# Kernel optimization log

Measured on AMD Instinct MI355X. Metric: run time of the kernel, lower is better.

Reference implementation:

```python
import jax, jax.numpy as jnp
import numpy as np

IN_F = 512
OUT_F = 512
TREES = 50
DEPTH = 10  # levels above leaves; 2^DEPTH leaves per tree


def _build_forest(T, D):
    """Forest of T perfect binary trees. Nodes laid out level-by-level (leaves first).
    Returns node_order [N], adjacency [E,2] (parent, child; children consecutive,
    left then right, edges sorted by parent), edge_order [E]."""
    per = 2 ** (D + 1) - 1
    no = np.zeros(per, np.int64)
    adj_parts, eo_parts = [], []
    start, prev = 0, None
    for l in range(D + 1):
        n_l = 2 ** (D - l)
        idx = np.arange(start, start + n_l, dtype=np.int64)
        no[idx] = l
        if l > 0:
            parents = np.repeat(idx, 2)          # each parent twice
            adj_parts.append(np.stack([parents, prev], 1))  # prev = 2*n_l children, pairs consecutive
            eo_parts.append(np.full(2 * n_l, l, np.int64))
        prev, start = idx, start + n_l
    adj = np.concatenate(adj_parts, 0)
    eo = np.concatenate(eo_parts, 0)
    offs = np.arange(T, dtype=np.int64) * per
    node_order = np.tile(no, T)
    adjacency = (adj[None] + offs[:, None, None]).reshape(-1, 2)
    edge_order = np.tile(eo, T)
    return node_order, adjacency, edge_order


def setup_inputs() -> dict:
    key = jax.random.key(0)
    ks = jax.random.split(key, 8)
    no, adj, eo = _build_forest(TREES, DEPTH)
    N = no.shape[0]
    s_in = 1.0 / np.sqrt(IN_F).astype(np.float32)
    s_h = 1.0 / np.sqrt(OUT_F).astype(np.float32)
    return {
        "features": jax.random.normal(ks[0], (N, IN_F), jnp.float32),
        "node_order": jnp.asarray(no),
        "adjacency_list": jnp.asarray(adj),
        "edge_order": jnp.asarray(eo),
        "W_iou_w": jax.random.normal(ks[1], (3 * OUT_F, IN_F), jnp.float32) * s_in,
        "W_iou_b": jax.random.normal(ks[2], (3 * OUT_F,), jnp.float32) * s_in,
        "U_iou_l": jax.random.normal(ks[3], (3 * OUT_F, OUT_F), jnp.float32) * s_h,
        "U_iou_r": jax.random.normal(ks[4], (3 * OUT_F, OUT_F), jnp.float32) * s_h,
        "W_f_w": jax.random.normal(ks[5], (OUT_F, IN_F), jnp.float32) * s_in,
        "W_f_b": jax.random.normal(ks[6], (OUT_F,), jnp.float32) * s_in,
        "U_f_l": jax.random.normal(ks[7], (OUT_F, OUT_F), jnp.float32) * s_h,
        "U_f_r": jax.random.normal(jax.random.fold_in(key, 99), (OUT_F, OUT_F), jnp.float32) * s_h,
    }


def reference(features, node_order, adjacency_list, edge_order,
              W_iou_w, W_iou_b, U_iou_l, U_iou_r, W_f_w, W_f_b, U_f_l, U_f_r):
    # Tree topology is static integer data: hoist it to numpy so per-level index
    # sets are concrete (the original torch code host-syncs the same way).
    no = np.asarray(node_order)
    ao = np.asarray(adjacency_list)
    eo = np.asarray(edge_order)
    N, H = features.shape[0], W_f_w.shape[0]
    h = jnp.zeros((N, H), features.dtype)
    c = jnp.zeros((N, H), features.dtype)
    for l in range(int(no.max()) + 1):
        nodes = jnp.asarray(np.nonzero(no == l)[0])   # parents at this level, sorted
        x = features[nodes]                            # [P, F]
        if l == 0:
            iou = x @ W_iou_w.T + W_iou_b
            i, o, u = jnp.split(iou, 3, axis=1)
            c_new = jax.nn.sigmoid(i) * jnp.tanh(u)
        else:
            e = ao[eo == l]                            # [2P, 2]; children consecutive per parent
            p_rep = jnp.asarray(e[:, 0])               # parent repeated per child
            children = jnp.asarray(e[:, 1])
            ch = h[children]                           # [2P, H]
            cc = c[children]                           # [2P, H]
            iou = (x @ W_iou_w.T + W_iou_b
                   + ch[0::2] @ U_iou_l.T              # left child h
                   + ch[1::2] @ U_iou_r.T)             # right child h
            i, o, u = jnp.split(iou, 3, axis=1)
            wf = features[p_rep] @ W_f_w.T + W_f_b     # [2P, H]
            f_l = jax.nn.sigmoid(wf + ch @ U_f_l.T)
            f_r = jax.nn.sigmoid(wf + ch @ U_f_r.T)
            fc = (f_l + f_r) * cc                      # [2P, H]
            c_new = jax.nn.sigmoid(i) * jnp.tanh(u) + fc.reshape(-1, 2, H).sum(1)
        h_new = jax.nn.sigmoid(o) * jnp.tanh(c_new)
        c = c.at[nodes].set(c_new)
        h = h.at[nodes].set(h_new)
    return h, c
```

## Files before the change

### kernel.cpp

```cpp
#include <hip/hip_runtime.h>
#include <hip/hip_bf16.h>

#define TREES_ 50
#define PER_ 2047
#define NN_ (TREES_ * PER_)
#define NINT_ (TREES_ * 1023)
#define NLEAF_ (TREES_ * 1024)

typedef __attribute__((ext_vector_type(8))) short s8v;
typedef __attribute__((ext_vector_type(4))) float f4v;

__device__ __forceinline__ unsigned short f2bf(float f) {
  union { float f; unsigned u; } v; v.f = f;
  unsigned r = v.u + 0x7FFFu + ((v.u >> 16) & 1u);
  return (unsigned short)(r >> 16);
}
__device__ __forceinline__ float bf2f(unsigned short s) {
  union { unsigned u; float f; } v; v.u = ((unsigned)s) << 16;
  return v.f;
}
__device__ __forceinline__ float sigm(float x) { return 1.f / (1.f + __expf(-x)); }
__device__ __forceinline__ float tanh_s(float x) {
  float ax = fabsf(x);
  float e = __expf(2.f * ax);
  float t = 1.f - 2.f / (e + 1.f);
  return copysignf(t, x);
}
__device__ __forceinline__ f4v fz4() { f4v z; z[0]=0.f; z[1]=0.f; z[2]=0.f; z[3]=0.f; return z; }

#if defined(__has_builtin)
#if __has_builtin(__builtin_amdgcn_global_load_lds)
#define HAS_GLD 1
#endif
#endif
__device__ __forceinline__ void gld16(const void* g, void* l) {
#ifdef HAS_GLD
  __builtin_amdgcn_global_load_lds(
      (const __attribute__((address_space(1))) unsigned int*)g,
      (__attribute__((address_space(3))) unsigned int*)l, 16, 0, 0);
#else
  *(s8v*)l = *(const s8v*)g;
#endif
}

__device__ __forceinline__ int xcd_swz(int bid, int nwg) {
  int q = nwg >> 3, r = nwg & 7, x = bid & 7, pos = bid >> 3;
  int base = (x < r) ? x * (q + 1) : r * (q + 1) + (x - r) * q;
  return base + pos;
}

#define LDS_BYTE(row, c16) ((row) * 128 + (((c16) ^ ((row) & 7)) << 4))

#define MFMA_STEP(Ap, Bp)                                                     \
  _Pragma("unroll") for (int kk = 0; kk < 2; ++kk) {                          \
    s8v af[4], bf_[4];                                                        \
    _Pragma("unroll") for (int i = 0; i < 4; ++i) {                           \
      int R = wr * 64 + i * 16 + lr;                                          \
      af[i] = *(const s8v*)((const char*)(Ap) + LDS_BYTE(R, kk * 4 + lg));    \
    }                                                                         \
    _Pragma("unroll") for (int j = 0; j < 4; ++j) {                           \
      int R = wc * 64 + j * 16 + lr;                                          \
      bf_[j] = *(const s8v*)((const char*)(Bp) + LDS_BYTE(R, kk * 4 + lg));   \
    }                                                                         \
    _Pragma("unroll") for (int i = 0; i < 4; ++i)                             \
      _Pragma("unroll") for (int j = 0; j < 4; ++j)                           \
        acc[i][j] = __builtin_amdgcn_mfma_f32_16x16x32_bf16(af[i], bf_[j],    \
                                                            acc[i][j], 0, 0, 0); \
  }

#define VMCNT8() asm volatile("s_waitcnt vmcnt(8)" ::: "memory")
#define VMCNT0() asm volatile("s_waitcnt vmcnt(0)" ::: "memory")
#define LGKM0()  asm volatile("s_waitcnt lgkmcnt(0)" ::: "memory")
#define SBAR()   __builtin_amdgcn_s_barrier()
#define SCHEDB() __builtin_amdgcn_sched_barrier(0)

#define PIPELINE(STAGEM, NT)                                       \
  STAGEM(0, 0)                                                     \
  STAGEM(1, 64)                                                    \
  {                                                                \
    int cur = 0;                                                   \
    for (int t = 0; t < (NT) - 1; ++t) {                           \
      VMCNT8(); SBAR();                                            \
      __builtin_amdgcn_s_setprio(1);                               \
      MFMA_STEP(AsB + cur * 8192, BsB + cur * 8192)                \
      __builtin_amdgcn_s_setprio(0);                               \
      LGKM0(); SCHEDB(); SBAR();                                   \
      if (t + 2 < (NT)) { STAGEM(cur, (t + 2) * 64) }              \
      cur ^= 1;                                                    \
    }                                                              \
    VMCNT0(); SBAR();                                              \
    MFMA_STEP(AsB + cur * 8192, BsB + cur * 8192)                  \
  }

__global__ __launch_bounds__(256) void feat2bf(const float* __restrict__ feat,
                                               unsigned short* __restrict__ FB) {
  long long i = (long long)blockIdx.x * 256 + threadIdx.x;
  if (i >= (long long)NN_ * 64) return;
  const float* src = feat + i * 8;
  float4 f0 = *(const float4*)src;
  float4 f1 = *(const float4*)(src + 4);
  s8v v;
  v[0] = (short)f2bf(f0.x); v[1] = (short)f2bf(f0.y);
  v[2] = (short)f2bf(f0.z); v[3] = (short)f2bf(f0.w);
  v[4] = (short)f2bf(f1.x); v[5] = (short)f2bf(f1.y);
  v[6] = (short)f2bf(f1.z); v[7] = (short)f2bf(f1.w);
  *(s8v*)(FB + i * 8) = v;
}

__global__ __launch_bounds__(256) void prep_weights(
    const float* __restrict__ Wiou, const float* __restrict__ Ul,
    const float* __restrict__ Ur,  const float* __restrict__ Wf,
    const float* __restrict__ Ufl, const float* __restrict__ Ufr,
    unsigned short* __restrict__ UCAT2, unsigned short* __restrict__ UFLR,
    unsigned short* __restrict__ WFB) {
  int i = blockIdx.x * 256 + threadIdx.x;
  if (i < 1536 * 1536) {
    int r = i / 1536, c = i - r * 1536;
    float v = (c < 512) ? Ul[r * 512 + c]
            : (c < 1024) ? Ur[r * 512 + (c - 512)]
                         : Wiou[r * 512 + (c - 1024)];
    UCAT2[i] = f2bf(v);
  }
  if (i < 1024 * 512) {
    int r = i >> 9, k = i & 511;
    int c = r >> 1, s = r & 1;
    UFLR[i] = f2bf(s ? Ufr[c * 512 + k] : Ufl[c * 512 + k]);
  }
  if (i < 512 * 512) WFB[i] = f2bf(Wf[i]);
}

__global__ __launch_bounds__(256) void pre_mm(
    const unsigned short* __restrict__ FB, const unsigned short* __restrict__ WFB,
    const unsigned short* __restrict__ UCAT2,
    const float* __restrict__ bfb, const float* __restrict__ biou,
    unsigned short* __restrict__ WF, unsigned short* __restrict__ LIOU,
    int nwgW, int nwgL) {
  __shared__ __align__(16) unsigned short AsB[2 * 128 * 64];
  __shared__ __align__(16) unsigned short BsB[2 * 128 * 64];
  const int tid = threadIdx.x;
  const int wid = tid >> 6, lane = tid & 63;
  const int wr = wid >> 1, wc = wid & 1;
  const int lr = lane & 15, lg = lane >> 4;
  f4v acc[4][4];
#pragma unroll
  for (int i = 0; i < 4; ++i)
#pragma unroll
    for (int j = 0; j < 4; ++j) acc[i][j] = fz4();

  const unsigned short* aA[4]; const unsigned short* aB[4];
  int tm, tn;
  const bool isW = (int)blockIdx.x < nwgW;
  if (isW) {
    const int swz = xcd_swz(blockIdx.x, nwgW);
    tn = swz & 3; tm = swz >> 2;
#pragma unroll
    for (int L = 0; L < 4; ++L) {
      int q = L * 256 + tid;
      int row = q >> 3, c16g = (q & 7) ^ (row & 7);
      int m = tm * 128 + row; if (m >= NINT_) m = NINT_ - 1;
      unsigned t = (unsigned)m / 1023u;
      int node = (int)t * 2047 + 1024 + (m - (int)t * 1023);
      aA[L] = FB + (size_t)node * 512 + c16g * 8;
      int n = tn * 128 + row;
      aB[L] = WFB + (size_t)n * 512 + c16g * 8;
    }
  } else {
    const int swz = xcd_swz((int)blockIdx.x - nwgW, nwgL);
    tn = swz % 12; tm = swz / 12;
#pragma unroll
    for (int L = 0; L < 4; ++L) {
      int q = L * 256 + tid;
      int row = q >> 3, c16g = (q & 7) ^ (row & 7);
      int m = tm * 128 + row;
      int node = (m >> 10) * 2047 + (m & 1023);
      aA[L] = FB + (size_t)node * 512 + c16g * 8;
      int n = tn * 128 + row;
      aB[L] = UCAT2 + (size_t)n * 1536 + 1024 + c16g * 8;
    }
  }
#define STAGE_P(bb, kofs)                                         \
  _Pragma("unroll") for (int L = 0; L < 4; ++L) {                 \
    int q = L * 256 + tid;                                        \
    gld16(aA[L] + (kofs), AsB + (bb) * 8192 + q * 8);             \
    gld16(aB[L] + (kofs), BsB + (bb) * 8192 + q * 8);             \
  }
  PIPELINE(STAGE_P, 8)

  if (isW) {
#pragma unroll
    for (int i = 0; i < 4; ++i)
#pragma unroll
      for (int j = 0; j < 4; ++j) {
        int n = tn * 128 + wc * 64 + j * 16 + lr;
        float bias = bfb[n];
#pragma unroll
        for (int r = 0; r < 4; ++r) {
          int m = tm * 128 + wr * 64 + i * 16 + lg * 4 + r;
          if (m < NINT_) WF[(size_t)m * 512 + n] = f2bf(acc[i][j][r] + bias);
        }
      }
  } else {
#pragma unroll
    for (int i = 0; i < 4; ++i)
#pragma unroll
      for (int j = 0; j < 4; ++j) {
        int n = tn * 128 + wc * 64 + j * 16 + lr;
        float bias = biou[n];
#pragma unroll
        for (int r = 0; r < 4; ++r) {
          int m = tm * 128 + wr * 64 + i * 16 + lg * 4 + r;
          LIOU[(size_t)m * 1536 + n] = f2bf(acc[i][j][r] + bias);
        }
      }
  }
}

__global__ __launch_bounds__(256) void leaf_ew(
    const unsigned short* __restrict__ LIOU,
    float* __restrict__ h_out, float* __restrict__ c_out,
    unsigned short* __restrict__ HB) {
  int idx = blockIdx.x * 256 + threadIdx.x;
  int r = idx >> 7;
  int c4 = (idx & 127) << 2;
  int g = (r >> 10) * 2047 + (r & 1023);
  const unsigned short* pr = LIOU + (size_t)r * 1536;
  ushort4 iv = *(const ushort4*)(pr + c4);
  ushort4 ov = *(const ushort4*)(pr + 512 + c4);
  ushort4 uv = *(const ushort4*)(pr + 1024 + c4);
  float4 hv, cv; ushort4 hb;
  float cc, hh;
  cc = sigm(bf2f(iv.x)) * tanh_s(bf2f(uv.x)); hh = sigm(bf2f(ov.x)) * tanh_s(cc);
  cv.x = cc; hv.x = hh; hb.x = f2bf(hh);
  cc = sigm(bf2f(iv.y)) * tanh_s(bf2f(uv.y)); hh = sigm(bf2f(ov.y)) * tanh_s(cc);
  cv.y = cc; hv.y = hh; hb.y = f2bf(hh);
  cc = sigm(bf2f(iv.z)) * tanh_s(bf2f(uv.z)); hh = sigm(bf2f(ov.z)) * tanh_s(cc);
  cv.z = cc; hv.z = hh; hb.z = f2bf(hh);
  cc = sigm(bf2f(iv.w)) * tanh_s(bf2f(uv.w)); hh = sigm(bf2f(ov.w)) * tanh_s(cc);
  cv.w = cc; hv.w = hh; hb.w = f2bf(hh);
  *(float4*)(h_out + (size_t)g * 512 + c4) = hv;
  *(float4*)(c_out + (size_t)g * 512 + c4) = cv;
  *(ushort4*)(HB + (size_t)g * 512 + c4) = hb;
}

__global__ __launch_bounds__(256) void lvl_gemm(
    const unsigned short* __restrict__ HB, const unsigned short* __restrict__ FB,
    const unsigned short* __restrict__ UFLR, const unsigned short* __restrict__ UCAT2,
    const unsigned short* __restrict__ WF, const float* __restrict__ biou,
    const float* __restrict__ c_out, float* __restrict__ h_out,
    unsigned short* __restrict__ IOU,
    int P, int shift, int start_l, int start_lm1, int nwg1, int nwg2) {
  __shared__ __align__(16) unsigned short AsB[2 * 128 * 64];
  __shared__ __align__(16) unsigned short BsB[2 * 128 * 64];
  const int tid = threadIdx.x;
  const int wid = tid >> 6, lane = tid & 63;
  const int wr = wid >> 1, wc = wid & 1;
  const int lr = lane & 15, lg = lane >> 4;
  const int pmask = (1 << shift) - 1;
  f4v acc[4][4];
#pragma unroll
  for (int i = 0; i < 4; ++i)
#pragma unroll
    for (int j = 0; j < 4; ++j) acc[i][j] = fz4();

  if ((int)blockIdx.x < nwg1) {
    const int swz = xcd_swz(blockIdx.x, nwg1);
    const int tn = swz & 7, tm = swz >> 3;
    const int M2 = 2 * P;
    const int cmask = (2 << shift) - 1;
    const unsigned short* aA[4]; const unsigned short* aB[4];
#pragma unroll
    for (int L = 0; L < 4; ++L) {
      int q = L * 256 + tid;
      int row = q >> 3, c16g = (q & 7) ^ (row & 7);
      int jg = tm * 128 + row; if (jg >= M2) jg = M2 - 1;
      int t = jg >> (shift + 1), idx = jg & cmask;
      aA[L] = HB + (size_t)(t * PER_ + start_lm1 + idx) * 512 + c16g * 8;
      int n = tn * 128 + row;
      aB[L] = UFLR + (size_t)n * 512 + c16g * 8;
    }
#define STAGE_G1(bb, kofs)                                        \
  _Pragma("unroll") for (int L = 0; L < 4; ++L) {                 \
    int q = L * 256 + tid;                                        \
    gld16(aA[L] + (kofs), AsB + (bb) * 8192 + q * 8);             \
    gld16(aB[L] + (kofs), BsB + (bb) * 8192 + q * 8);             \
  }
    PIPELINE(STAGE_G1, 8)

    const int soff = start_l - 1024;
#pragma unroll
    for (int i = 0; i < 4; ++i) {
      int mbase = tm * 128 + wr * 64 + i * 16;
#pragma unroll
      for (int j = 0; j < 4; ++j) {
        int nn = tn * 128 + wc * 64 + j * 16 + lr;
        int hcol = nn >> 1;
        float fc[4];
#pragma unroll
        for (int r = 0; r < 4; ++r) {
          int m = mbase + lg * 4 + r;
          int mm = (m < M2) ? m : 0;
          int pidx = mm >> 1;
          int t = pidx >> shift, k = pidx & pmask;
          float wf = bf2f(WF[(size_t)(t * 1023 + soff + k) * 512 + hcol]);
          float sv = sigm(wf + acc[i][j][r]);
          float spair = sv + __shfl_xor(sv, 1, 64);
          float cc = 0.f;
          if ((lr & 1) == 0)
            cc = c_out[(size_t)(t * PER_ + start_lm1 + (mm & cmask)) * 512 + hcol];
          fc[r] = spair * cc;
        }
        if ((lr & 1) == 0) {
          int p0 = (mbase >> 1) + lg * 2;
          if (p0 < P) {
            int t0 = p0 >> shift, k0p = p0 & pmask;
            h_out[(size_t)(t0 * PER_ + start_l + k0p) * 512 + hcol] = fc[0] + fc[1];
          }
          int p1 = (mbase >> 1) + lg * 2 + 1;
          if (p1 < P) {
            int t1 = p1 >> shift, k1p = p1 & pmask;
            h_out[(size_t)(t1 * PER_ + start_l + k1p) * 512 + hcol] = fc[2] + fc[3];
          }
        }
      }
    }
  } else {
    const int swz = xcd_swz((int)blockIdx.x - nwg1, nwg2);
    const int tn = swz % 12, tm = swz / 12;
    const unsigned short* aHB[4]; const unsigned short* aFB[4];
    const unsigned short* aB[4];
#pragma unroll
    for (int L = 0; L < 4; ++L) {
      int q = L * 256 + tid;
      int row = q >> 3, c16g = (q & 7) ^ (row & 7);
      int p = tm * 128 + row; if (p >= P) p = P - 1;
      int t = p >> shift, kp = p & pmask;
      aHB[L] = HB + (size_t)(t * PER_ + start_lm1) * 512 + (size_t)kp * 1024 + c16g * 8;
      aFB[L] = FB + (size_t)(t * PER_ + start_l + kp) * 512 + c16g * 8 - 1024;
      int n = tn * 128 + row;
      aB[L] = UCAT2 + (size_t)n * 1536 + c16g * 8;
    }
#define STAGE_G2(bb, kofs)                                                    \
  _Pragma("unroll") for (int L = 0; L < 4; ++L) {                             \
    int q = L * 256 + tid;                                                    \
    const unsigned short* srcA =                                              \
        ((kofs) < 1024) ? aHB[L] + (kofs) : aFB[L] + (kofs);                  \
    gld16(srcA, AsB + (bb) * 8192 + q * 8);                                   \
    gld16(aB[L] + (kofs), BsB + (bb) * 8192 + q * 8);                         \
  }
    PIPELINE(STAGE_G2, 24)
#pragma unroll
    for (int i = 0; i < 4; ++i)
#pragma unroll
      for (int j = 0; j < 4; ++j) {
        int n = tn * 128 + wc * 64 + j * 16 + lr;
        float bias = biou[n];
#pragma unroll
        for (int r = 0; r < 4; ++r) {
          int m = tm * 128 + wr * 64 + i * 16 + lg * 4 + r;
          if (m < P) IOU[(size_t)m * 1536 + n] = f2bf(acc[i][j][r] + bias);
        }
      }
  }
}

__global__ __launch_bounds__(256) void g3_kernel(
    const unsigned short* __restrict__ IOU,
    float* __restrict__ h_out, float* __restrict__ c_out,
    unsigned short* __restrict__ HB, int P, int shift, int start_l) {
  int idx = blockIdx.x * 256 + threadIdx.x;
  int p = idx >> 7;
  if (p >= P) return;
  int c4 = (idx & 127) << 2;
  int t = p >> shift, k = p & ((1 << shift) - 1);
  size_t pg = (size_t)(t * PER_ + start_l + k);
  const unsigned short* ir = IOU + (size_t)p * 1536;
  ushort4 iv = *(const ushort4*)(ir + c4);
  ushort4 ov = *(const ushort4*)(ir + 512 + c4);
  ushort4 uv = *(const ushort4*)(ir + 1024 + c4);
  float4 fcs = *(const float4*)(h_out + pg * 512 + c4);
  float4 hv, cv; ushort4 hb;
  float cc, hh;
  cc = sigm(bf2f(iv.x)) * tanh_s(bf2f(uv.x)) + fcs.x; hh = sigm(bf2f(ov.x)) * tanh_s(cc);
  cv.x = cc; hv.x = hh; hb.x = f2bf(hh);
  cc = sigm(bf2f(iv.y)) * tanh_s(bf2f(uv.y)) + fcs.y; hh = sigm(bf2f(ov.y)) * tanh_s(cc);
  cv.y = cc; hv.y = hh; hb.y = f2bf(hh);
  cc = sigm(bf2f(iv.z)) * tanh_s(bf2f(uv.z)) + fcs.z; hh = sigm(bf2f(ov.z)) * tanh_s(cc);
  cv.z = cc; hv.z = hh; hb.z = f2bf(hh);
  cc = sigm(bf2f(iv.w)) * tanh_s(bf2f(uv.w)) + fcs.w; hh = sigm(bf2f(ov.w)) * tanh_s(cc);
  cv.w = cc; hv.w = hh; hb.w = f2bf(hh);
  *(float4*)(h_out + pg * 512 + c4) = hv;
  *(float4*)(c_out + pg * 512 + c4) = cv;
  *(ushort4*)(HB + pg * 512 + c4) = hb;
}

__global__ void fill_sentinel(float* out, int n) {
  int i = blockIdx.x * 256 + threadIdx.x;
  if (i < n) out[i] = 12345.0f;
}

extern "C" void kernel_launch(void* const* d_in, const int* in_sizes, int n_in,
                              void* d_out, int out_size, void* d_ws, size_t ws_size,
                              hipStream_t stream) {
  (void)in_sizes; (void)n_in; (void)out_size;
  const float* feat = (const float*)d_in[0];
  const float* Wiou = (const float*)d_in[4];
  const float* biou = (const float*)d_in[5];
  const float* Ul   = (const float*)d_in[6];
  const float* Ur   = (const float*)d_in[7];
  const float* Wf   = (const float*)d_in[8];
  const float* bfb  = (const float*)d_in[9];
  const float* Ufl  = (const float*)d_in[10];
  const float* Ufr  = (const float*)d_in[11];
  float* h_out = (float*)d_out;
  float* c_out = h_out + (size_t)NN_ * 512;

  const size_t OFF_HB   = 0;
  const size_t SZ_HB    = (size_t)NN_ * 512 * 2;
  const size_t OFF_FB   = OFF_HB + SZ_HB;
  const size_t SZ_FB    = (size_t)NN_ * 512 * 2;
  const size_t OFF_WFm  = OFF_FB + SZ_FB;
  const size_t SZ_WF    = (size_t)NINT_ * 512 * 2;
  const size_t OFF_UC2  = OFF_WFm + SZ_WF;
  const size_t SZ_UC2   = 1536 * 1536 * 2;
  const size_t OFF_UFLR = OFF_UC2 + SZ_UC2;
  const size_t SZ_UFLR  = 1024 * 512 * 2;
  const size_t OFF_WFB  = OFF_UFLR + SZ_UFLR;
  const size_t SZ_WFB   = 512 * 512 * 2;
  const size_t OFF_LIOU = OFF_WFB + SZ_WFB;
  const size_t SZ_LIOU  = (size_t)NLEAF_ * 1536 * 2;
  const size_t NEEDED   = OFF_LIOU + SZ_LIOU;

  if (ws_size < NEEDED) {
    int n = 2 * NN_ * 512;
    fill_sentinel<<<(n + 255) / 256, 256, 0, stream>>>((float*)d_out, n);
    return;
  }

  char* ws = (char*)d_ws;
  unsigned short* HB    = (unsigned short*)(ws + OFF_HB);
  unsigned short* FB    = (unsigned short*)(ws + OFF_FB);
  unsigned short* WF    = (unsigned short*)(ws + OFF_WFm);
  unsigned short* UCAT2 = (unsigned short*)(ws + OFF_UC2);
  unsigned short* UFLR  = (unsigned short*)(ws + OFF_UFLR);
  unsigned short* WFB   = (unsigned short*)(ws + OFF_WFB);
  unsigned short* LIOU  = (unsigned short*)(ws + OFF_LIOU);
  unsigned short* IOU   = (unsigned short*)(ws + OFF_LIOU);

  prep_weights<<<9216, 256, 0, stream>>>(Wiou, Ul, Ur, Wf, Ufl, Ufr,
                                         UCAT2, UFLR, WFB);
  feat2bf<<<(NN_ * 64 + 255) / 256, 256, 0, stream>>>(feat, FB);
  {
    int nwgW = ((NINT_ + 127) / 128) * 4;
    int nwgL = (NLEAF_ / 128) * 12;
    pre_mm<<<nwgW + nwgL, 256, 0, stream>>>(FB, WFB, UCAT2, bfb, biou,
                                            WF, LIOU, nwgW, nwgL);
  }
  leaf_ew<<<(NLEAF_ * 128) / 256, 256, 0, stream>>>(LIOU, h_out, c_out, HB);

  for (int l = 1; l <= 10; ++l) {
    int shift = 10 - l;
    int P = TREES_ << shift;
    int start_l   = 2048 - (1 << (11 - l));
    int start_lm1 = 2048 - (1 << (12 - l));
    int nwg1 = ((2 * P + 127) / 128) * 8;
    int nwg2 = ((P + 127) / 128) * 12;
    lvl_gemm<<<nwg1 + nwg2, 256, 0, stream>>>(HB, FB, UFLR, UCAT2, WF, biou,
                                              c_out, h_out, IOU,
                                              P, shift, start_l, start_lm1,
                                              nwg1, nwg2);
    int g3b = (P * 128 + 255) / 256;
    g3_kernel<<<g3b, 256, 0, stream>>>(IOU, h_out, c_out, HB, P, shift, start_l);
  }
}
```

Measured before the change: 1.460 ms.

## Precompute W_iou·x for internal nodes, use 256x256 tiles, move forget gates to epilogue kernel

The x@W_iou term for all internal nodes is now computed once in the prologue GEMM (XIOU), so per-level GEMMs only contract over the child hidden states (K=1024 instead of 1536). GEMM tiles grow to 256x256 with 512 threads and a simpler double-buffered pipeline using __syncthreads. The forget-gate sigmoid and cell reduction move out of the GEMM epilogue into the elementwise kernel, which reads a bf16 F buffer. This trades less per-level MFMA work for more workspace, extra memory traffic through F and XIOU, and fewer workgroups on the small upper levels.

```diff
diff --git a/kernel.cpp b/kernel.cpp
--- a/kernel.cpp
+++ b/kernel.cpp
@@ -9,6 +9,7 @@
 
 typedef __attribute__((ext_vector_type(8))) short s8v;
 typedef __attribute__((ext_vector_type(4))) float f4v;
+typedef __attribute__((ext_vector_type(4))) unsigned short u4v;
 
 __device__ __forceinline__ unsigned short f2bf(float f) {
   union { float f; unsigned u; } v; v.f = f;
@@ -51,45 +52,34 @@
 
 #define LDS_BYTE(row, c16) ((row) * 128 + (((c16) ^ ((row) & 7)) << 4))
 
-#define MFMA_STEP(Ap, Bp)                                                     \
+#define MFMA256(Ap, Bp)                                                       \
   _Pragma("unroll") for (int kk = 0; kk < 2; ++kk) {                          \
-    s8v af[4], bf_[4];                                                        \
-    _Pragma("unroll") for (int i = 0; i < 4; ++i) {                           \
-      int R = wr * 64 + i * 16 + lr;                                          \
+    s8v af[8], bf_[4];                                                        \
+    _Pragma("unroll") for (int i = 0; i < 8; ++i) {                           \
+      int R = wm * 128 + i * 16 + lr;                                         \
       af[i] = *(const s8v*)((const char*)(Ap) + LDS_BYTE(R, kk * 4 + lg));    \
     }                                                                         \
     _Pragma("unroll") for (int j = 0; j < 4; ++j) {                           \
-      int R = wc * 64 + j * 16 + lr;                                          \
+      int R = wn * 64 + j * 16 + lr;                                          \
       bf_[j] = *(const s8v*)((const char*)(Bp) + LDS_BYTE(R, kk * 4 + lg));   \
     }                                                                         \
-    _Pragma("unroll") for (int i = 0; i < 4; ++i)                             \
+    _Pragma("unroll") for (int i = 0; i < 8; ++i)                             \
       _Pragma("unroll") for (int j = 0; j < 4; ++j)                           \
         acc[i][j] = __builtin_amdgcn_mfma_f32_16x16x32_bf16(af[i], bf_[j],    \
                                                             acc[i][j], 0, 0, 0); \
   }
 
-#define VMCNT8() asm volatile("s_waitcnt vmcnt(8)" ::: "memory")
-#define VMCNT0() asm volatile("s_waitcnt vmcnt(0)" ::: "memory")
-#define LGKM0()  asm volatile("s_waitcnt lgkmcnt(0)" ::: "memory")
-#define SBAR()   __builtin_amdgcn_s_barrier()
-#define SCHEDB() __builtin_amdgcn_sched_barrier(0)
-
-#define PIPELINE(STAGEM, NT)                                       \
+#define PIPE2(STAGEM, NT)                                          \
   STAGEM(0, 0)                                                     \
-  STAGEM(1, 64)                                                    \
+  __syncthreads();                                                 \
   {                                                                \
     int cur = 0;                                                   \
-    for (int t = 0; t < (NT) - 1; ++t) {                           \
-      VMCNT8(); SBAR();                                            \
-      __builtin_amdgcn_s_setprio(1);                               \
-      MFMA_STEP(AsB + cur * 8192, BsB + cur * 8192)                \
-      __builtin_amdgcn_s_setprio(0);                               \
-      LGKM0(); SCHEDB(); SBAR();                                   \
-      if (t + 2 < (NT)) { STAGEM(cur, (t + 2) * 64) }              \
+    for (int t = 0; t < (NT); ++t) {                               \
+      if (t + 1 < (NT)) { STAGEM(cur ^ 1, (t + 1) * 64) }          \
+      MFMA256(AsB + cur * 16384, BsB + cur * 16384)                \
+      __syncthreads();                                             \
       cur ^= 1;                                                    \
     }                                                              \
-    VMCNT0(); SBAR();                                              \
-    MFMA_STEP(AsB + cur * 8192, BsB + cur * 8192)                  \
   }
 
 __global__ __launch_bounds__(256) void feat2bf(const float* __restrict__ feat,
@@ -111,15 +101,14 @@
     const float* __restrict__ Wiou, const float* __restrict__ Ul,
     const float* __restrict__ Ur,  const float* __restrict__ Wf,
     const float* __restrict__ Ufl, const float* __restrict__ Ufr,
-    unsigned short* __restrict__ UCAT2, unsigned short* __restrict__ UFLR,
-    unsigned short* __restrict__ WFB) {
+    unsigned short* __restrict__ WIOUB, unsigned short* __restrict__ UCAT3,
+    unsigned short* __restrict__ UFLR, unsigned short* __restrict__ WFB) {
   int i = blockIdx.x * 256 + threadIdx.x;
-  if (i < 1536 * 1536) {
-    int r = i / 1536, c = i - r * 1536;
-    float v = (c < 512) ? Ul[r * 512 + c]
-            : (c < 1024) ? Ur[r * 512 + (c - 512)]
-                         : Wiou[r * 512 + (c - 1024)];
-    UCAT2[i] = f2bf(v);
+  if (i < 1536 * 512) WIOUB[i] = f2bf(Wiou[i]);
+  if (i < 1536 * 1024) {
+    int r = i >> 10, c = i & 1023;
+    float v = (c < 512) ? Ul[r * 512 + c] : Ur[r * 512 + (c - 512)];
+    UCAT3[i] = f2bf(v);
   }
   if (i < 1024 * 512) {
     int r = i >> 9, k = i & 511;
@@ -129,90 +118,82 @@
   if (i < 512 * 512) WFB[i] = f2bf(Wf[i]);
 }
 
-__global__ __launch_bounds__(256) void pre_mm(
+__global__ __launch_bounds__(512, 2) void pre_mm(
     const unsigned short* __restrict__ FB, const unsigned short* __restrict__ WFB,
-    const unsigned short* __restrict__ UCAT2,
+    const unsigned short* __restrict__ WIOUB,
     const float* __restrict__ bfb, const float* __restrict__ biou,
     unsigned short* __restrict__ WF, unsigned short* __restrict__ LIOU,
-    int nwgW, int nwgL) {
-  __shared__ __align__(16) unsigned short AsB[2 * 128 * 64];
-  __shared__ __align__(16) unsigned short BsB[2 * 128 * 64];
+    unsigned short* __restrict__ XIOU, int nwgA, int nwgB, int nwgC) {
+  __shared__ __align__(16) unsigned short AsB[2 * 256 * 64];
+  __shared__ __align__(16) unsigned short BsB[2 * 256 * 64];
   const int tid = threadIdx.x;
   const int wid = tid >> 6, lane = tid & 63;
-  const int wr = wid >> 1, wc = wid & 1;
+  const int wm = wid >> 2, wn = wid & 3;
   const int lr = lane & 15, lg = lane >> 4;
-  f4v acc[4][4];
-#pragma unroll
-  for (int i = 0; i < 4; ++i)
+  f4v acc[8][4];
+#pragma unroll
+  for (int i = 0; i < 8; ++i)
 #pragma unroll
     for (int j = 0; j < 4; ++j) acc[i][j] = fz4();
 
   const unsigned short* aA[4]; const unsigned short* aB[4];
-  int tm, tn;
-  const bool isW = (int)blockIdx.x < nwgW;
-  if (isW) {
-    const int swz = xcd_swz(blockIdx.x, nwgW);
-    tn = swz & 3; tm = swz >> 2;
-#pragma unroll
-    for (int L = 0; L < 4; ++L) {
-      int q = L * 256 + tid;
-      int row = q >> 3, c16g = (q & 7) ^ (row & 7);
-      int m = tm * 128 + row; if (m >= NINT_) m = NINT_ - 1;
-      unsigned t = (unsigned)m / 1023u;
-      int node = (int)t * 2047 + 1024 + (m - (int)t * 1023);
-      aA[L] = FB + (size_t)node * 512 + c16g * 8;
-      int n = tn * 128 + row;
-      aB[L] = WFB + (size_t)n * 512 + c16g * 8;
+  int tm, tn, which;
+  if ((int)blockIdx.x < nwgA) {
+    which = 0;
+    int swz = xcd_swz(blockIdx.x, nwgA);
+    tn = swz & 1; tm = swz >> 1;
+  } else if ((int)blockIdx.x < nwgA + nwgB) {
+    which = 1;
+    int swz = xcd_swz((int)blockIdx.x - nwgA, nwgB);
+    tn = swz % 6; tm = swz / 6;
+  } else {
+    which = 2;
+    int swz = xcd_swz((int)blockIdx.x - nwgA - nwgB, nwgC);
+    tn = swz % 6; tm = swz / 6;
+  }
+#pragma unroll
+  for (int L = 0; L < 4; ++L) {
+    int q = L * 512 + tid;
+    int row = q >> 3, c16g = (q & 7) ^ (row & 7);
+    int m = tm * 256 + row;
+    int node;
+    if (which == 1) {
+      node = (m >> 10) * 2047 + (m & 1023);
+    } else {
+      if (m >= NINT_) m = NINT_ - 1;
+      int t = (unsigned)m / 1023u;
+      node = t * 2047 + 1024 + (m - t * 1023);
     }
-  } else {
-    const int swz = xcd_swz((int)blockIdx.x - nwgW, nwgL);
-    tn = swz % 12; tm = swz / 12;
-#pragma unroll
-    for (int L = 0; L < 4; ++L) {
-      int q = L * 256 + tid;
-      int row = q >> 3, c16g = (q & 7) ^ (row & 7);
-      int m = tm * 128 + row;
-      int node = (m >> 10) * 2047 + (m & 1023);
-      aA[L] = FB + (size_t)node * 512 + c16g * 8;
-      int n = tn * 128 + row;
-      aB[L] = UCAT2 + (size_t)n * 1536 + 1024 + c16g * 8;
-    }
+    aA[L] = FB + (size_t)node * 512 + c16g * 8;
+    int n = tn * 256 + row;
+    aB[L] = (which == 0 ? WFB : WIOUB) + (size_t)n * 512 + c16g * 8;
   }
 #define STAGE_P(bb, kofs)                                         \
   _Pragma("unroll") for (int L = 0; L < 4; ++L) {                 \
-    int q = L * 256 + tid;                                        \
-    gld16(aA[L] + (kofs), AsB + (bb) * 8192 + q * 8);             \
-    gld16(aB[L] + (kofs), BsB + (bb) * 8192 + q * 8);             \
-  }
-  PIPELINE(STAGE_P, 8)
-
-  if (isW) {
-#pragma unroll
-    for (int i = 0; i < 4; ++i)
-#pragma unroll
-      for (int j = 0; j < 4; ++j) {
-        int n = tn * 128 + wc * 64 + j * 16 + lr;
-        float bias = bfb[n];
-#pragma unroll
-        for (int r = 0; r < 4; ++r) {
-          int m = tm * 128 + wr * 64 + i * 16 + lg * 4 + r;
+    int q = L * 512 + tid;                                        \
+    gld16(aA[L] + (kofs), AsB + (bb) * 16384 + q * 8);            \
+    gld16(aB[L] + (kofs), BsB + (bb) * 16384 + q * 8);            \
+  }
+  PIPE2(STAGE_P, 8)
+
+#pragma unroll
+  for (int i = 0; i < 8; ++i)
+#pragma unroll
+    for (int j = 0; j < 4; ++j) {
+      int n = tn * 256 + wn * 64 + j * 16 + lr;
+      float bias = (which == 0) ? bfb[n] : biou[n];
+#pragma unroll
+      for (int r = 0; r < 4; ++r) {
+        int m = tm * 256 + wm * 128 + i * 16 + lg * 4 + r;
+        if (which == 0) {
           if (m < NINT_) WF[(size_t)m * 512 + n] = f2bf(acc[i][j][r] + bias);
+        } else if (which == 1) {
+          LIOU[(size_t)m * 1536 + n] = f2bf(acc[i][j][r] + bias);
+        } else {
+          if (m < NINT_) XIOU[(size_t)m * 1536 + n] = f2bf(acc[i][j][r] + bias);
         }
       }
-  } else {
-#pragma unroll
-    for (int i = 0; i < 4; ++i)
-#pragma unroll
-      for (int j = 0; j < 4; ++j) {
-        int n = tn * 128 + wc * 64 + j * 16 + lr;
-        float bias = biou[n];
-#pragma unroll
-        for (int r = 0; r < 4; ++r) {
-          int m = tm * 128 + wr * 64 + i * 16 + lg * 4 + r;
-          LIOU[(size_t)m * 1536 + n] = f2bf(acc[i][j][r] + bias);
-        }
-      }
-  }
+    }
 }
 
 __global__ __launch_bounds__(256) void leaf_ew(
@@ -224,173 +205,151 @@
   int c4 = (idx & 127) << 2;
   int g = (r >> 10) * 2047 + (r & 1023);
   const unsigned short* pr = LIOU + (size_t)r * 1536;
-  ushort4 iv = *(const ushort4*)(pr + c4);
-  ushort4 ov = *(const ushort4*)(pr + 512 + c4);
-  ushort4 uv = *(const ushort4*)(pr + 1024 + c4);
-  float4 hv, cv; ushort4 hb;
-  float cc, hh;
-  cc = sigm(bf2f(iv.x)) * tanh_s(bf2f(uv.x)); hh = sigm(bf2f(ov.x)) * tanh_s(cc);
-  cv.x = cc; hv.x = hh; hb.x = f2bf(hh);
-  cc = sigm(bf2f(iv.y)) * tanh_s(bf2f(uv.y)); hh = sigm(bf2f(ov.y)) * tanh_s(cc);
-  cv.y = cc; hv.y = hh; hb.y = f2bf(hh);
-  cc = sigm(bf2f(iv.z)) * tanh_s(bf2f(uv.z)); hh = sigm(bf2f(ov.z)) * tanh_s(cc);
-  cv.z = cc; hv.z = hh; hb.z = f2bf(hh);
-  cc = sigm(bf2f(iv.w)) * tanh_s(bf2f(uv.w)); hh = sigm(bf2f(ov.w)) * tanh_s(cc);
-  cv.w = cc; hv.w = hh; hb.w = f2bf(hh);
-  *(float4*)(h_out + (size_t)g * 512 + c4) = hv;
-  *(float4*)(c_out + (size_t)g * 512 + c4) = cv;
-  *(ushort4*)(HB + (size_t)g * 512 + c4) = hb;
-}
-
-__global__ __launch_bounds__(256) void lvl_gemm(
-    const unsigned short* __restrict__ HB, const unsigned short* __restrict__ FB,
-    const unsigned short* __restrict__ UFLR, const unsigned short* __restrict__ UCAT2,
-    const unsigned short* __restrict__ WF, const float* __restrict__ biou,
-    const float* __restrict__ c_out, float* __restrict__ h_out,
-    unsigned short* __restrict__ IOU,
-    int P, int shift, int start_l, int start_lm1, int nwg1, int nwg2) {
-  __shared__ __align__(16) unsigned short AsB[2 * 128 * 64];
-  __shared__ __align__(16) unsigned short BsB[2 * 128 * 64];
+  u4v iv = *(const u4v*)(pr + c4);
+  u4v ov = *(const u4v*)(pr + 512 + c4);
+  u4v uv = *(const u4v*)(pr + 1024 + c4);
+  f4v hv, cv; u4v hb;
+#pragma unroll
+  for (int x = 0; x < 4; ++x) {
+    float cc = sigm(bf2f(iv[x])) * tanh_s(bf2f(uv[x]));
+    float hh = sigm(bf2f(ov[x])) * tanh_s(cc);
+    cv[x] = cc; hv[x] = hh; hb[x] = f2bf(hh);
+  }
+  *(f4v*)(h_out + (size_t)g * 512 + c4) = hv;
+  *(f4v*)(c_out + (size_t)g * 512 + c4) = cv;
+  *(u4v*)(HB + (size_t)g * 512 + c4) = hb;
+}
+
+__global__ __launch_bounds__(512, 2) void g12(
+    const unsigned short* __restrict__ HB, const unsigned short* __restrict__ UFLR,
+    const unsigned short* __restrict__ UCAT3, unsigned short* __restrict__ XIOU,
+    unsigned short* __restrict__ F,
+    int P, int shift, int start_lm1, int soff, int nwg1, int nwg2) {
+  __shared__ __align__(16) unsigned short AsB[2 * 256 * 64];
+  __shared__ __align__(16) unsigned short BsB[2 * 256 * 64];
   const int tid = threadIdx.x;
   const int wid = tid >> 6, lane = tid & 63;
-  const int wr = wid >> 1, wc = wid & 1;
+  const int wm = wid >> 2, wn = wid & 3;
   const int lr = lane & 15, lg = lane >> 4;
   const int pmask = (1 << shift) - 1;
-  f4v acc[4][4];
-#pragma unroll
-  for (int i = 0; i < 4; ++i)
+  f4v acc[8][4];
+#pragma unroll
+  for (int i = 0; i < 8; ++i)
 #pragma unroll
     for (int j = 0; j < 4; ++j) acc[i][j] = fz4();
 
   if ((int)blockIdx.x < nwg1) {
     const int swz = xcd_swz(blockIdx.x, nwg1);
-    const int tn = swz & 7, tm = swz >> 3;
+    const int tn = swz & 3, tm = swz >> 2;
     const int M2 = 2 * P;
     const int cmask = (2 << shift) - 1;
     const unsigned short* aA[4]; const unsigned short* aB[4];
 #pragma unroll
     for (int L = 0; L < 4; ++L) {
-      int q = L * 256 + tid;
+      int q = L * 512 + tid;
       int row = q >> 3, c16g = (q & 7) ^ (row & 7);
-      int jg = tm * 128 + row; if (jg >= M2) jg = M2 - 1;
-      int t = jg >> (shift + 1), idx = jg & cmask;
-      aA[L] = HB + (size_t)(t * PER_ + start_lm1 + idx) * 512 + c16g * 8;
-      int n = tn * 128 + row;
+      int jg = tm * 256 + row; if (jg >= M2) jg = M2 - 1;
+      int t = jg >> (shift + 1);
+      aA[L] = HB + (size_t)(t * PER_ + start_lm1 + (jg & cmask)) * 512 + c16g * 8;
+      int n = tn * 256 + row;
       aB[L] = UFLR + (size_t)n * 512 + c16g * 8;
     }
 #define STAGE_G1(bb, kofs)                                        \
   _Pragma("unroll") for (int L = 0; L < 4; ++L) {                 \
-    int q = L * 256 + tid;                                        \
-    gld16(aA[L] + (kofs), AsB + (bb) * 8192 + q * 8);             \
-    gld16(aB[L] + (kofs), BsB + (bb) * 8192 + q * 8);             \
-  }
-    PIPELINE(STAGE_G1, 8)
-
-    const int soff = start_l - 1024;
-#pragma unroll
-    for (int i = 0; i < 4; ++i) {
-      int mbase = tm * 128 + wr * 64 + i * 16;
+    int q = L * 512 + tid;                                        \
+    gld16(aA[L] + (kofs), AsB + (bb) * 16384 + q * 8);            \
+    gld16(aB[L] + (kofs), BsB + (bb) * 16384 + q * 8);            \
+  }
+    PIPE2(STAGE_G1, 8)
+#pragma unroll
+    for (int i = 0; i < 8; ++i)
 #pragma unroll
       for (int j = 0; j < 4; ++j) {
-        int nn = tn * 128 + wc * 64 + j * 16 + lr;
-        int hcol = nn >> 1;
-        float fc[4];
+        int n = tn * 256 + wn * 64 + j * 16 + lr;
 #pragma unroll
         for (int r = 0; r < 4; ++r) {
-          int m = mbase + lg * 4 + r;
-          int mm = (m < M2) ? m : 0;
-          int pidx = mm >> 1;
-          int t = pidx >> shift, k = pidx & pmask;
-          float wf = bf2f(WF[(size_t)(t * 1023 + soff + k) * 512 + hcol]);
-          float sv = sigm(wf + acc[i][j][r]);
-          float spair = sv + __shfl_xor(sv, 1, 64);
-          float cc = 0.f;
-          if ((lr & 1) == 0)
-            cc = c_out[(size_t)(t * PER_ + start_lm1 + (mm & cmask)) * 512 + hcol];
-          fc[r] = spair * cc;
+          int jrow = tm * 256 + wm * 128 + i * 16 + lg * 4 + r;
+          if (jrow < M2) F[(size_t)jrow * 1024 + n] = f2bf(acc[i][j][r]);
         }
-        if ((lr & 1) == 0) {
-          int p0 = (mbase >> 1) + lg * 2;
-          if (p0 < P) {
-            int t0 = p0 >> shift, k0p = p0 & pmask;
-            h_out[(size_t)(t0 * PER_ + start_l + k0p) * 512 + hcol] = fc[0] + fc[1];
-          }
-          int p1 = (mbase >> 1) + lg * 2 + 1;
-          if (p1 < P) {
-            int t1 = p1 >> shift, k1p = p1 & pmask;
-            h_out[(size_t)(t1 * PER_ + start_l + k1p) * 512 + hcol] = fc[2] + fc[3];
+      }
+  } else {
+    const int swz = xcd_swz((int)blockIdx.x - nwg1, nwg2);
+    const int tn = swz % 6, tm = swz / 6;
+    const unsigned short* aA[4]; const unsigned short* aB[4];
+#pragma unroll
+    for (int L = 0; L < 4; ++L) {
+      int q = L * 512 + tid;
+      int row = q >> 3, c16g = (q & 7) ^ (row & 7);
+      int p = tm * 256 + row; if (p >= P) p = P - 1;
+      int t = p >> shift, kp = p & pmask;
+      aA[L] = HB + (size_t)(t * PER_ + start_lm1) * 512 + (size_t)kp * 1024 + c16g * 8;
+      int n = tn * 256 + row;
+      aB[L] = UCAT3 + (size_t)n * 1024 + c16g * 8;
+    }
+#define STAGE_G2(bb, kofs)                                        \
+  _Pragma("unroll") for (int L = 0; L < 4; ++L) {                 \
+    int q = L * 512 + tid;                                        \
+    gld16(aA[L] + (kofs), AsB + (bb) * 16384 + q * 8);            \
+    gld16(aB[L] + (kofs), BsB + (bb) * 16384 + q * 8);            \
+  }
+    PIPE2(STAGE_G2, 16)
+#pragma unroll
+    for (int i = 0; i < 8; ++i)
+#pragma unroll
+      for (int j = 0; j < 4; ++j) {
+        int n = tn * 256 + wn * 64 + j * 16 + lr;
+#pragma unroll
+        for (int r = 0; r < 4; ++r) {
+          int p = tm * 256 + wm * 128 + i * 16 + lg * 4 + r;
+          if (p < P) {
+            int t = p >> shift, k = p & pmask;
+            size_t mi = (size_t)(t * 1023 + soff + k);
+            size_t o = mi * 1536 + n;
+            XIOU[o] = f2bf(bf2f(XIOU[o]) + acc[i][j][r]);
           }
         }
       }
-    }
-  } else {
-    const int swz = xcd_swz((int)blockIdx.x - nwg1, nwg2);
-    const int tn = swz % 12, tm = swz / 12;
-    const unsigned short* aHB[4]; const unsigned short* aFB[4];
-    const unsigned short* aB[4];
-#pragma unroll
-    for (int L = 0; L < 4; ++L) {
-      int q = L * 256 + tid;
-      int row = q >> 3, c16g = (q & 7) ^ (row & 7);
-      int p = tm * 128 + row; if (p >= P) p = P - 1;
-      int t = p >> shift, kp = p & pmask;
-      aHB[L] = HB + (size_t)(t * PER_ + start_lm1) * 512 + (size_t)kp * 1024 + c16g * 8;
-      aFB[L] = FB + (size_t)(t * PER_ + start_l + kp) * 512 + c16g * 8 - 1024;
-      int n = tn * 128 + row;
-      aB[L] = UCAT2 + (size_t)n * 1536 + c16g * 8;
-    }
-#define STAGE_G2(bb, kofs)                                                    \
-  _Pragma("unroll") for (int L = 0; L < 4; ++L) {                             \
-    int q = L * 256 + tid;                                                    \
-    const unsigned short* srcA =                                              \
-        ((kofs) < 1024) ? aHB[L] + (kofs) : aFB[L] + (kofs);                  \
-    gld16(srcA, AsB + (bb) * 8192 + q * 8);                                   \
-    gld16(aB[L] + (kofs), BsB + (bb) * 8192 + q * 8);                         \
-  }
-    PIPELINE(STAGE_G2, 24)
-#pragma unroll
-    for (int i = 0; i < 4; ++i)
-#pragma unroll
-      for (int j = 0; j < 4; ++j) {
-        int n = tn * 128 + wc * 64 + j * 16 + lr;
-        float bias = biou[n];
-#pragma unroll
-        for (int r = 0; r < 4; ++r) {
-          int m = tm * 128 + wr * 64 + i * 16 + lg * 4 + r;
-          if (m < P) IOU[(size_t)m * 1536 + n] = f2bf(acc[i][j][r] + bias);
-        }
-      }
-  }
-}
-
-__global__ __launch_bounds__(256) void g3_kernel(
-    const unsigned short* __restrict__ IOU,
+  }
+}
+
+__global__ __launch_bounds__(256) void g3_big(
+    const unsigned short* __restrict__ F, const unsigned short* __restrict__ WF,
+    const unsigned short* __restrict__ XIOU,
     float* __restrict__ h_out, float* __restrict__ c_out,
-    unsigned short* __restrict__ HB, int P, int shift, int start_l) {
+    unsigned short* __restrict__ HB,
+    int P, int shift, int start_l, int start_lm1, int soff) {
   int idx = blockIdx.x * 256 + threadIdx.x;
   int p = idx >> 7;
   if (p >= P) return;
   int c4 = (idx & 127) << 2;
   int t = p >> shift, k = p & ((1 << shift) - 1);
   size_t pg = (size_t)(t * PER_ + start_l + k);
-  const unsigned short* ir = IOU + (size_t)p * 1536;
-  ushort4 iv = *(const ushort4*)(ir + c4);
-  ushort4 ov = *(const ushort4*)(ir + 512 + c4);
-  ushort4 uv = *(const ushort4*)(ir + 1024 + c4);
-  float4 fcs = *(const float4*)(h_out + pg * 512 + c4);
-  float4 hv, cv; ushort4 hb;
-  float cc, hh;
-  cc = sigm(bf2f(iv.x)) * tanh_s(bf2f(uv.x)) + fcs.x; hh = sigm(bf2f(ov.x)) * tanh_s(cc);
-  cv.x = cc; hv.x = hh; hb.x = f2bf(hh);
-  cc = sigm(bf2f(iv.y)) * tanh_s(bf2f(uv.y)) + fcs.y; hh = sigm(bf2f(ov.y)) * tanh_s(cc);
-  cv.y = cc; hv.y = hh; hb.y = f2bf(hh);
-  cc = sigm(bf2f(iv.z)) * tanh_s(bf2f(uv.z)) + fcs.z; hh = sigm(bf2f(ov.z)) * tanh_s(cc);
-  cv.z = cc; hv.z = hh; hb.z = f2bf(hh);
-  cc = sigm(bf2f(iv.w)) * tanh_s(bf2f(uv.w)) + fcs.w; hh = sigm(bf2f(ov.w)) * tanh_s(cc);
-  cv.w = cc; hv.w = hh; hb.w = f2bf(hh);
-  *(float4*)(h_out + pg * 512 + c4) = hv;
-  *(float4*)(c_out + pg * 512 + c4) = cv;
-  *(ushort4*)(HB + pg * 512 + c4) = hb;
+  size_t mi = (size_t)(t * 1023 + soff + k);
+  size_t cg0 = (size_t)(t * PER_ + start_lm1 + 2 * k);
+  const unsigned short* xr = XIOU + mi * 1536;
+  u4v iv = *(const u4v*)(xr + c4);
+  u4v ov = *(const u4v*)(xr + 512 + c4);
+  u4v uv = *(const u4v*)(xr + 1024 + c4);
+  u4v wfv = *(const u4v*)(WF + mi * 512 + c4);
+  s8v f0 = *(const s8v*)(F + (size_t)(2 * p) * 1024 + 2 * c4);
+  s8v f1 = *(const s8v*)(F + (size_t)(2 * p + 1) * 1024 + 2 * c4);
+  f4v cc0 = *(const f4v*)(c_out + cg0 * 512 + c4);
+  f4v cc1 = *(const f4v*)(c_out + (cg0 + 1) * 512 + c4);
+  f4v hv, cv; u4v hb;
+#pragma unroll
+  for (int x = 0; x < 4; ++x) {
+    float wf = bf2f(wfv[x]);
+    float fc = (sigm(wf + bf2f((unsigned short)f0[2 * x])) +
+                sigm(wf + bf2f((unsigned short)f0[2 * x + 1]))) * cc0[x]
+             + (sigm(wf + bf2f((unsigned short)f1[2 * x])) +
+                sigm(wf + bf2f((unsigned short)f1[2 * x + 1]))) * cc1[x];
+    float cvv = sigm(bf2f(iv[x])) * tanh_s(bf2f(uv[x])) + fc;
+    float hvv = sigm(bf2f(ov[x])) * tanh_s(cvv);
+    cv[x] = cvv; hv[x] = hvv; hb[x] = f2bf(hvv);
+  }
+  *(f4v*)(h_out + pg * 512 + c4) = hv;
+  *(f4v*)(c_out + pg * 512 + c4) = cv;
+  *(u4v*)(HB + pg * 512 + c4) = hb;
 }
 
 __global__ void fill_sentinel(float* out, int n) {
@@ -414,21 +373,25 @@
   float* h_out = (float*)d_out;
   float* c_out = h_out + (size_t)NN_ * 512;
 
-  const size_t OFF_HB   = 0;
-  const size_t SZ_HB    = (size_t)NN_ * 512 * 2;
-  const size_t OFF_FB   = OFF_HB + SZ_HB;
-  const size_t SZ_FB    = (size_t)NN_ * 512 * 2;
-  const size_t OFF_WFm  = OFF_FB + SZ_FB;
-  const size_t SZ_WF    = (size_t)NINT_ * 512 * 2;
-  const size_t OFF_UC2  = OFF_WFm + SZ_WF;
-  const size_t SZ_UC2   = 1536 * 1536 * 2;
-  const size_t OFF_UFLR = OFF_UC2 + SZ_UC2;
-  const size_t SZ_UFLR  = 1024 * 512 * 2;
-  const size_t OFF_WFB  = OFF_UFLR + SZ_UFLR;
-  const size_t SZ_WFB   = 512 * 512 * 2;
-  const size_t OFF_LIOU = OFF_WFB + SZ_WFB;
-  const size_t SZ_LIOU  = (size_t)NLEAF_ * 1536 * 2;
-  const size_t NEEDED   = OFF_LIOU + SZ_LIOU;
+  const size_t OFF_HB    = 0;
+  const size_t SZ_HB     = (size_t)NN_ * 512 * 2;
+  const size_t OFF_FB    = OFF_HB + SZ_HB;
+  const size_t SZ_FB     = (size_t)NN_ * 512 * 2;
+  const size_t OFF_WFm   = OFF_FB + SZ_FB;
+  const size_t SZ_WF     = (size_t)NINT_ * 512 * 2;
+  const size_t OFF_WIOUB = OFF_WFm + SZ_WF;
+  const size_t SZ_WIOUB  = 1536 * 512 * 2;
+  const size_t OFF_UC3   = OFF_WIOUB + SZ_WIOUB;
+  const size_t SZ_UC3    = 1536 * 1024 * 2;
+  const size_t OFF_UFLR  = OFF_UC3 + SZ_UC3;
+  const size_t SZ_UFLR   = 1024 * 512 * 2;
+  const size_t OFF_WFB   = OFF_UFLR + SZ_UFLR;
+  const size_t SZ_WFB    = 512 * 512 * 2;
+  const size_t OFF_XIOU  = OFF_WFB + SZ_WFB;
+  const size_t SZ_XIOU   = (size_t)NINT_ * 1536 * 2;
+  const size_t OFF_LF    = OFF_XIOU + SZ_XIOU;
+  const size_t SZ_LF     = (size_t)NLEAF_ * 1536 * 2;
+  const size_t NEEDED    = OFF_LF + SZ_LF;
 
   if (ws_size < NEEDED) {
     int n = 2 * NN_ * 512;
@@ -440,20 +403,24 @@
   unsigned short* HB    = (unsigned short*)(ws + OFF_HB);
   unsigned short* FB    = (unsigned short*)(ws + OFF_FB);
   unsigned short* WF    = (unsigned short*)(ws + OFF_WFm);
-  unsigned short* UCAT2 = (unsigned short*)(ws + OFF_UC2);
+  unsigned short* WIOUB = (unsigned short*)(ws + OFF_WIOUB);
+  unsigned short* UCAT3 = (unsigned short*)(ws + OFF_UC3);
   unsigned short* UFLR  = (unsigned short*)(ws + OFF_UFLR);
   unsigned short* WFB   = (unsigned short*)(ws + OFF_WFB);
-  unsigned short* LIOU  = (unsigned short*)(ws + OFF_LIOU);
-  unsigned short* IOU   = (unsigned short*)(ws + OFF_LIOU);
-
-  prep_weights<<<9216, 256, 0, stream>>>(Wiou, Ul, Ur, Wf, Ufl, Ufr,
-                                         UCAT2, UFLR, WFB);
+  unsigned short* XIOU  = (unsigned short*)(ws + OFF_XIOU);
+  unsigned short* LIOU  = (unsigned short*)(ws + OFF_LF);
+  unsigned short* F     = (unsigned short*)(ws + OFF_LF);
+
+  prep_weights<<<6144, 256, 0, stream>>>(Wiou, Ul, Ur, Wf, Ufl, Ufr,
+                                         WIOUB, UCAT3, UFLR, WFB);
   feat2bf<<<(NN_ * 64 + 255) / 256, 256, 0, stream>>>(feat, FB);
   {
-    int nwgW = ((NINT_ + 127) / 128) * 4;
-    int nwgL = (NLEAF_ / 128) * 12;
-    pre_mm<<<nwgW + nwgL, 256, 0, stream>>>(FB, WFB, UCAT2, bfb, biou,
-                                            WF, LIOU, nwgW, nwgL);
+    int nwgA = 200 * 2;
+    int nwgB = 200 * 6;
+    int nwgC = 200 * 6;
+    pre_mm<<<nwgA + nwgB + nwgC, 512, 0, stream>>>(FB, WFB, WIOUB, bfb, biou,
+                                                   WF, LIOU, XIOU,
+                                                   nwgA, nwgB, nwgC);
   }
   leaf_ew<<<(NLEAF_ * 128) / 256, 256, 0, stream>>>(LIOU, h_out, c_out, HB);
 
@@ -462,13 +429,13 @@
     int P = TREES_ << shift;
     int start_l   = 2048 - (1 << (11 - l));
     int start_lm1 = 2048 - (1 << (12 - l));
-    int nwg1 = ((2 * P + 127) / 128) * 8;
-    int nwg2 = ((P + 127) / 128) * 12;
-    lvl_gemm<<<nwg1 + nwg2, 256, 0, stream>>>(HB, FB, UFLR, UCAT2, WF, biou,
-                                              c_out, h_out, IOU,
-                                              P, shift, start_l, start_lm1,
-                                              nwg1, nwg2);
+    int soff = start_l - 1024;
+    int nwg1 = ((2 * P + 255) / 256) * 4;
+    int nwg2 = ((P + 255) / 256) * 6;
+    g12<<<nwg1 + nwg2, 512, 0, stream>>>(HB, UFLR, UCAT3, XIOU, F,
+                                         P, shift, start_lm1, soff, nwg1, nwg2);
     int g3b = (P * 128 + 255) / 256;
-    g3_kernel<<<g3b, 256, 0, stream>>>(IOU, h_out, c_out, HB, P, shift, start_l);
-  }
-}
+    g3_big<<<g3b, 256, 0, stream>>>(F, WF, XIOU, h_out, c_out, HB,
+                                    P, shift, start_l, start_lm1, soff);
+  }
+}
```

New measurement: 1.812 ms. 24.1% more time.
